# Kernel optimization log

Hardware: AMD Instinct MI355X
Metric: run time of the kernel (lower is better)

The kernel has to match this reference:

```python
import jax, jax.numpy as jnp
import numpy as np

EPS = 1e-5

def ln(x, w, b):
    mu = jnp.mean(x, axis=-1, keepdims=True)
    var = jnp.mean(jnp.square(x - mu), axis=-1, keepdims=True)
    return (x - mu) * jax.lax.rsqrt(var + EPS) * w + b

def setup_inputs() -> dict:
    key = jax.random.key(0)
    ks = jax.random.split(key, 4)
    B, H, W, C = 8, 224, 224, 96
    Cout = 2 * C  # 192
    x = jax.random.normal(ks[0], (B, H, W, C), dtype=jnp.float32)
    saliency_map = jax.random.uniform(ks[1], (B, H, W), dtype=jnp.float32)
    # PatchMerging reduction: Linear(4C -> 2C, bias=False), xavier_uniform init
    limit = float(np.sqrt(6.0 / (4 * C + Cout)))
    merge_w = jax.random.uniform(ks[2], (Cout, 4 * C), minval=-limit, maxval=limit, dtype=jnp.float32)
    return {
        "x": x,
        "saliency_map": saliency_map,
        "merge_w": merge_w,
        "merge_norm_w": jnp.ones((4 * C,), jnp.float32),
        "merge_norm_b": jnp.zeros((4 * C,), jnp.float32),
        "vss_norm_w": jnp.ones((Cout,), jnp.float32),
        "vss_norm_b": jnp.zeros((Cout,), jnp.float32),
        "asram_norm_w": jnp.ones((Cout,), jnp.float32),
        "asram_norm_b": jnp.zeros((Cout,), jnp.float32),
        "final_norm_w": jnp.ones((Cout,), jnp.float32),
        "final_norm_b": jnp.zeros((Cout,), jnp.float32),
    }

def reference(x, saliency_map, merge_w, merge_norm_w, merge_norm_b,
              vss_norm_w, vss_norm_b, asram_norm_w, asram_norm_b,
              final_norm_w, final_norm_b):
    # --- PatchMerging: [B,H,W,C] -> [B,H/2,W/2,2C] ---
    x0 = x[:, 0::2, 0::2, :]
    x1 = x[:, 1::2, 0::2, :]
    x2 = x[:, 0::2, 1::2, :]
    x3 = x[:, 1::2, 1::2, :]
    xm = jnp.concatenate([x0, x1, x2, x3], axis=-1)          # [B,H/2,W/2,4C]
    xm = ln(xm, merge_norm_w, merge_norm_b)
    xs = jnp.einsum('bhwi,oi->bhwo', xm, merge_w)            # [B,H/2,W/2,2C]
    # saliency adaptation (bilinear resize, align_corners=False); mock ASRAM ignores it
    B, Hn, Wn, _ = xs.shape
    _sal = jax.image.resize(saliency_map[:, None], (B, 1, Hn, Wn), method='bilinear')
    del _sal  # unused by mock ASRAM, kept for fidelity of the dataflow
    # --- Mock DualVSSBlock: x + LayerNorm(x) ---
    xv = xs + ln(xs, vss_norm_w, vss_norm_b)
    # --- Mock ASRAM: LayerNorm over channels (permute round-trip is a no-op here) ---
    xa = ln(xv, asram_norm_w, asram_norm_b)
    # --- Final LayerNorm ---
    return ln(xa, final_norm_w, final_norm_b)
```

## Files before the change

kernel.cpp:

```cpp
#include <hip/hip_runtime.h>
#include <cstdint>
#include <cstddef>

typedef float f32x4  __attribute__((ext_vector_type(4)));
typedef short bf16x8 __attribute__((ext_vector_type(8)));
typedef int   i32x4  __attribute__((ext_vector_type(4)));

#define LN_EPS 1e-5f

static __device__ __forceinline__ unsigned short f2bf(float f) {
    unsigned int u = __float_as_uint(f);
    u += 0x7fffu + ((u >> 16) & 1u);
    return (unsigned short)(u >> 16);
}
static __device__ __forceinline__ float bf2f(unsigned short h) {
    return __uint_as_float(((unsigned int)h) << 16);
}

__global__ void prep_w_kernel(const float* __restrict__ W,
                              unsigned short* __restrict__ wsh) {
    int o = blockIdx.x * 256 + threadIdx.x;
    if (o >= 192 * 384) return;
    int j    = o & 7;
    int lane = (o >> 3) & 63;
    int t    = o >> 9;
    int nf   = t % 12;
    int kk   = t / 12;
    int n = nf * 16 + (lane & 15);
    int k = kk * 32 + (lane >> 4) * 8 + j;
    wsh[o] = f2bf(W[n * 384 + k]);
}

template <bool USE_WS>
__global__ __launch_bounds__(256, 3)
void fused_kernel(const float* __restrict__ x,
                  const unsigned short* __restrict__ wsh,
                  const float* __restrict__ Wf,
                  const float* __restrict__ mw, const float* __restrict__ mb,
                  const float* __restrict__ vw, const float* __restrict__ vb,
                  const float* __restrict__ aw, const float* __restrict__ ab,
                  const float* __restrict__ fw, const float* __restrict__ fb,
                  float* __restrict__ out) {
    __shared__ __align__(16) unsigned char lds[49152];

    const int tid = threadIdx.x;
    const int r   = tid >> 3;
    const int u   = tid & 7;
    const int q   = u >> 1;
    const int hh  = u & 1;

    const int wv = tid >> 6;
    const int l  = tid & 63;
    const int g  = l >> 4;
    const int cl = l & 15;

    {
        const int R   = blockIdx.x * 32 + r;
        const int b   = R / 12544;
        const int rem = R - b * 12544;
        const int h2  = rem / 112;
        const int w2  = rem - h2 * 112;
        const int h   = 2 * h2 + (q & 1);
        const int w   = 2 * w2 + (q >> 1);
        const f32x4* src = (const f32x4*)(x + (((size_t)b * 224 + h) * 224 + w) * 96 + hh * 48);
        f32x4 v[12];
        #pragma unroll
        for (int i = 0; i < 12; i++) v[i] = src[i];

        float s = 0.f;
        #pragma unroll
        for (int i = 0; i < 12; i++) {
            #pragma unroll
            for (int e = 0; e < 4; e++) s += v[i][e];
        }
        s += __shfl_xor(s, 1); s += __shfl_xor(s, 2); s += __shfl_xor(s, 4);
        const float mu = s * (1.f / 384.f);
        float sd = 0.f;
        #pragma unroll
        for (int i = 0; i < 12; i++) {
            #pragma unroll
            for (int e = 0; e < 4; e++) { float d = v[i][e] - mu; sd += d * d; }
        }
        sd += __shfl_xor(sd, 1); sd += __shfl_xor(sd, 2); sd += __shfl_xor(sd, 4);
        const float rs = rsqrtf(sd * (1.f / 384.f) + LN_EPS);

        const f32x4* mwv = (const f32x4*)(mw + q * 96 + hh * 48);
        const f32x4* mbv = (const f32x4*)(mb + q * 96 + hh * 48);
        #pragma unroll
        for (int p = 0; p < 6; p++) {
            union { unsigned short u16[8]; i32x4 v4; } ph, pl;
            #pragma unroll
            for (int half = 0; half < 2; half++) {
                const int i = 2 * p + half;
                f32x4 w4 = mwv[i], b4 = mbv[i];
                #pragma unroll
                for (int e = 0; e < 4; e++) {
                    float a = (v[i][e] - mu) * rs * w4[e] + b4[e];
                    unsigned short hi = f2bf(a);
                    ph.u16[4 * half + e] = hi;
                    pl.u16[4 * half + e] = f2bf(a - bf2f(hi));
                }
            }
            const int slot = 6 * u + p;
            const int boff = (slot * 16) ^ ((r & 7) << 4);
            *(i32x4*)(&lds[r * 768 + boff])         = ph.v4;
            *(i32x4*)(&lds[24576 + r * 768 + boff]) = pl.v4;
        }
    }
    __syncthreads();

    f32x4 acc[2][3];
    #pragma unroll
    for (int mf = 0; mf < 2; mf++)
        #pragma unroll
        for (int t = 0; t < 3; t++) acc[mf][t] = (f32x4){0.f, 0.f, 0.f, 0.f};

    if (USE_WS) {
        #pragma unroll
        for (int half = 0; half < 2; half++) {
            bf16x8 B[6][3];
            #pragma unroll
            for (int kx = 0; kx < 6; kx++) {
                const int kk = 6 * half + kx;
                const bf16x8* bp = (const bf16x8*)wsh + ((kk * 12 + 3 * wv) * 64 + l);
                B[kx][0] = bp[0]; B[kx][1] = bp[64]; B[kx][2] = bp[128];
            }
            #pragma unroll
            for (int kx = 0; kx < 6; kx++) {
                asm volatile("" : "+v"(B[kx][0]), "+v"(B[kx][1]), "+v"(B[kx][2]));
            }
            #pragma unroll
            for (int kx = 0; kx < 6; kx++) {
                const int kk = 6 * half + kx;
                #pragma unroll
                for (int mf = 0; mf < 2; mf++) {
                    const int row  = 16 * mf + cl;
                    const int boff = (kk * 64 + g * 16) ^ ((row & 7) << 4);
                    bf16x8 afh = *(const bf16x8*)(&lds[row * 768 + boff]);
                    bf16x8 afl = *(const bf16x8*)(&lds[24576 + row * 768 + boff]);
                    #pragma unroll
                    for (int t = 0; t < 3; t++) {
                        acc[mf][t] = __builtin_amdgcn_mfma_f32_16x16x32_bf16(afh, B[kx][t], acc[mf][t], 0, 0, 0);
                        acc[mf][t] = __builtin_amdgcn_mfma_f32_16x16x32_bf16(afl, B[kx][t], acc[mf][t], 0, 0, 0);
                    }
                }
            }
        }
    } else {
        #pragma unroll
        for (int kk = 0; kk < 12; kk++) {
            bf16x8 bh[3];
            #pragma unroll
            for (int t = 0; t < 3; t++) {
                const int n = (3 * wv + t) * 16 + cl;
                const float* wp = Wf + n * 384 + kk * 32 + g * 8;
                f32x4 lo = *(const f32x4*)wp;
                f32x4 hi4 = *(const f32x4*)(wp + 4);
                bf16x8 hbb;
                #pragma unroll
                for (int e = 0; e < 4; e++) {
                    hbb[e] = (short)f2bf(lo[e]); hbb[4 + e] = (short)f2bf(hi4[e]);
                }
                bh[t] = hbb;
            }
            #pragma unroll
            for (int mf = 0; mf < 2; mf++) {
                const int row  = 16 * mf + cl;
                const int boff = (kk * 64 + g * 16) ^ ((row & 7) << 4);
                bf16x8 afh = *(const bf16x8*)(&lds[row * 768 + boff]);
                bf16x8 afl = *(const bf16x8*)(&lds[24576 + row * 768 + boff]);
                #pragma unroll
                for (int t = 0; t < 3; t++) {
                    acc[mf][t] = __builtin_amdgcn_mfma_f32_16x16x32_bf16(afh, bh[t], acc[mf][t], 0, 0, 0);
                    acc[mf][t] = __builtin_amdgcn_mfma_f32_16x16x32_bf16(afl, bh[t], acc[mf][t], 0, 0, 0);
                }
            }
        }
    }
    __syncthreads();

    {
        float* xsl = (float*)lds;
        #pragma unroll
        for (int mf = 0; mf < 2; mf++)
            #pragma unroll
            for (int t = 0; t < 3; t++) {
                const int col = 48 * wv + 16 * t + cl;
                #pragma unroll
                for (int rg = 0; rg < 4; rg++) {
                    const int row = 16 * mf + 4 * g + rg;
                    xsl[row * 196 + col] = acc[mf][t][rg];
                }
            }
    }
    __syncthreads();

    {
        const float* rowp = (const float*)lds + r * 196 + u * 24;
        float vv[24];
        #pragma unroll
        for (int i = 0; i < 6; i++) {
            f32x4 t4 = *(const f32x4*)(rowp + 4 * i);
            #pragma unroll
            for (int e = 0; e < 4; e++) vv[4 * i + e] = t4[e];
        }
        float s1 = 0.f;
        #pragma unroll
        for (int i = 0; i < 24; i++) s1 += vv[i];
        s1 += __shfl_xor(s1, 1); s1 += __shfl_xor(s1, 2); s1 += __shfl_xor(s1, 4);
        const float mu1 = s1 * (1.f / 192.f);
        float d1 = 0.f;
        #pragma unroll
        for (int i = 0; i < 24; i++) { float d = vv[i] - mu1; d1 += d * d; }
        d1 += __shfl_xor(d1, 1); d1 += __shfl_xor(d1, 2); d1 += __shfl_xor(d1, 4);
        const float r1 = rsqrtf(d1 * (1.f / 192.f) + LN_EPS);

        const f32x4* vwv = (const f32x4*)(vw + u * 24);
        const f32x4* vbv = (const f32x4*)(vb + u * 24);
        float s2 = 0.f;
        #pragma unroll
        for (int i = 0; i < 6; i++) {
            f32x4 w4 = vwv[i], b4 = vbv[i];
            #pragma unroll
            for (int e = 0; e < 4; e++) {
                float xs0 = vv[4 * i + e];
                float xv0 = xs0 + (xs0 - mu1) * r1 * w4[e] + b4[e];
                vv[4 * i + e] = xv0;
                s2 += xv0;
            }
        }
        s2 += __shfl_xor(s2, 1); s2 += __shfl_xor(s2, 2); s2 += __shfl_xor(s2, 4);
        const float mu2 = s2 * (1.f / 192.f);
        float d2 = 0.f;
        #pragma unroll
        for (int i = 0; i < 24; i++) { float d = vv[i] - mu2; d2 += d * d; }
        d2 += __shfl_xor(d2, 1); d2 += __shfl_xor(d2, 2); d2 += __shfl_xor(d2, 4);
        const float r2 = rsqrtf(d2 * (1.f / 192.f) + LN_EPS);

        const f32x4* awv = (const f32x4*)(aw + u * 24);
        const f32x4* abv = (const f32x4*)(ab + u * 24);
        float s3 = 0.f;
        #pragma unroll
        for (int i = 0; i < 6; i++) {
            f32x4 w4 = awv[i], b4 = abv[i];
            #pragma unroll
            for (int e = 0; e < 4; e++) {
                float xa0 = (vv[4 * i + e] - mu2) * r2 * w4[e] + b4[e];
                vv[4 * i + e] = xa0;
                s3 += xa0;
            }
        }
        s3 += __shfl_xor(s3, 1); s3 += __shfl_xor(s3, 2); s3 += __shfl_xor(s3, 4);
        const float mu3 = s3 * (1.f / 192.f);
        float d3 = 0.f;
        #pragma unroll
        for (int i = 0; i < 24; i++) { float d = vv[i] - mu3; d3 += d * d; }
        d3 += __shfl_xor(d3, 1); d3 += __shfl_xor(d3, 2); d3 += __shfl_xor(d3, 4);
        const float r3 = rsqrtf(d3 * (1.f / 192.f) + LN_EPS);

        const f32x4* fwv = (const f32x4*)(fw + u * 24);
        const f32x4* fbv = (const f32x4*)(fb + u * 24);
        float* op = out + (size_t)(blockIdx.x * 32 + r) * 192 + u * 24;
        #pragma unroll
        for (int i = 0; i < 6; i++) {
            f32x4 w4 = fwv[i], b4 = fbv[i];
            f32x4 o4;
            #pragma unroll
            for (int e = 0; e < 4; e++)
                o4[e] = (vv[4 * i + e] - mu3) * r3 * w4[e] + b4[e];
            *(f32x4*)(op + 4 * i) = o4;
        }
    }
}

extern "C" void kernel_launch(void* const* d_in, const int* in_sizes, int n_in,
                              void* d_out, int out_size, void* d_ws, size_t ws_size,
                              hipStream_t stream) {
    const float* x  = (const float*)d_in[0];
    const float* W  = (const float*)d_in[2];
    const float* mw = (const float*)d_in[3];
    const float* mb = (const float*)d_in[4];
    const float* vw = (const float*)d_in[5];
    const float* vb = (const float*)d_in[6];
    const float* aw = (const float*)d_in[7];
    const float* ab = (const float*)d_in[8];
    const float* fw = (const float*)d_in[9];
    const float* fb = (const float*)d_in[10];
    float* out = (float*)d_out;

    const int rows   = 8 * 112 * 112;
    const int blocks = rows / 32;

    unsigned short* wsh = (unsigned short*)d_ws;

    if (ws_size >= (size_t)(192 * 384 * 2)) {
        prep_w_kernel<<<288, 256, 0, stream>>>(W, wsh);
        fused_kernel<true><<<blocks, 256, 0, stream>>>(x, wsh, W, mw, mb, vw, vb,
                                                       aw, ab, fw, fb, out);
    } else {
        fused_kernel<false><<<blocks, 256, 0, stream>>>(x, wsh, W, mw, mb, vw, vb,
                                                        aw, ab, fw, fb, out);
    }
}
```

Baseline: 87.70 us.

## Fold merge LayerNorm affine into GEMM weights and apply normalization post-GEMM

The merge LayerNorm gamma is folded into the bf16 weights, and per-output constants (W·gamma, W·beta) are precomputed by a new small kernel. Raw x is split into hi/lo bf16 and written to LDS before the mean/variance are computed, so the LDS store no longer waits on the reduction. Normalization is applied after the GEMM as rs*(acc - mu*s2) + c0. This trades an extra tiny kernel launch and a possible precision change (cancellation on raw, un-centered inputs) for less per-element work before the GEMM. The bf16 conversion is also switched to the HIP intrinsic.

```diff
diff --git a/kernel.cpp b/kernel.cpp
--- a/kernel.cpp
+++ b/kernel.cpp
@@ -1,4 +1,5 @@
 #include <hip/hip_runtime.h>
+#include <hip/hip_bf16.h>
 #include <cstdint>
 #include <cstddef>
 
@@ -9,15 +10,16 @@
 #define LN_EPS 1e-5f
 
 static __device__ __forceinline__ unsigned short f2bf(float f) {
-    unsigned int u = __float_as_uint(f);
-    u += 0x7fffu + ((u >> 16) & 1u);
-    return (unsigned short)(u >> 16);
+    __hip_bfloat16 h = __float2bfloat16(f);
+    union { __hip_bfloat16 b; unsigned short u; } cv; cv.b = h;
+    return cv.u;
 }
 static __device__ __forceinline__ float bf2f(unsigned short h) {
     return __uint_as_float(((unsigned int)h) << 16);
 }
 
 __global__ void prep_w_kernel(const float* __restrict__ W,
+                              const float* __restrict__ g,
                               unsigned short* __restrict__ wsh) {
     int o = blockIdx.x * 256 + threadIdx.x;
     if (o >= 192 * 384) return;
@@ -28,13 +30,27 @@
     int kk   = t / 12;
     int n = nf * 16 + (lane & 15);
     int k = kk * 32 + (lane >> 4) * 8 + j;
-    wsh[o] = f2bf(W[n * 384 + k]);
+    wsh[o] = f2bf(g[k] * W[n * 384 + k]);
+}
+
+__global__ void prep_sc_kernel(const float* __restrict__ W,
+                               const float* __restrict__ g,
+                               const float* __restrict__ b,
+                               float* __restrict__ s2,
+                               float* __restrict__ c0) {
+    int o = threadIdx.x;
+    if (o >= 192) return;
+    const float* wr = W + o * 384;
+    float a = 0.f, c = 0.f;
+    for (int i = 0; i < 384; i++) { float w = wr[i]; a += g[i] * w; c += b[i] * w; }
+    s2[o] = a; c0[o] = c;
 }
 
 template <bool USE_WS>
 __global__ __launch_bounds__(256, 3)
 void fused_kernel(const float* __restrict__ x,
                   const unsigned short* __restrict__ wsh,
+                  const float* __restrict__ s2p, const float* __restrict__ c0p,
                   const float* __restrict__ Wf,
                   const float* __restrict__ mw, const float* __restrict__ mb,
                   const float* __restrict__ vw, const float* __restrict__ vb,
@@ -53,6 +69,8 @@
     const int l  = tid & 63;
     const int g  = l >> 4;
     const int cl = l & 15;
+
+    float mu = 0.f, rs = 0.f;
 
     {
         const int R   = blockIdx.x * 32 + r;
@@ -67,44 +85,82 @@
         #pragma unroll
         for (int i = 0; i < 12; i++) v[i] = src[i];
 
-        float s = 0.f;
-        #pragma unroll
-        for (int i = 0; i < 12; i++) {
-            #pragma unroll
-            for (int e = 0; e < 4; e++) s += v[i][e];
-        }
-        s += __shfl_xor(s, 1); s += __shfl_xor(s, 2); s += __shfl_xor(s, 4);
-        const float mu = s * (1.f / 384.f);
-        float sd = 0.f;
-        #pragma unroll
-        for (int i = 0; i < 12; i++) {
-            #pragma unroll
-            for (int e = 0; e < 4; e++) { float d = v[i][e] - mu; sd += d * d; }
-        }
-        sd += __shfl_xor(sd, 1); sd += __shfl_xor(sd, 2); sd += __shfl_xor(sd, 4);
-        const float rs = rsqrtf(sd * (1.f / 384.f) + LN_EPS);
-
-        const f32x4* mwv = (const f32x4*)(mw + q * 96 + hh * 48);
-        const f32x4* mbv = (const f32x4*)(mb + q * 96 + hh * 48);
-        #pragma unroll
-        for (int p = 0; p < 6; p++) {
-            union { unsigned short u16[8]; i32x4 v4; } ph, pl;
-            #pragma unroll
-            for (int half = 0; half < 2; half++) {
-                const int i = 2 * p + half;
-                f32x4 w4 = mwv[i], b4 = mbv[i];
-                #pragma unroll
-                for (int e = 0; e < 4; e++) {
-                    float a = (v[i][e] - mu) * rs * w4[e] + b4[e];
-                    unsigned short hi = f2bf(a);
-                    ph.u16[4 * half + e] = hi;
-                    pl.u16[4 * half + e] = f2bf(a - bf2f(hi));
-                }
-            }
-            const int slot = 6 * u + p;
-            const int boff = (slot * 16) ^ ((r & 7) << 4);
-            *(i32x4*)(&lds[r * 768 + boff])         = ph.v4;
-            *(i32x4*)(&lds[24576 + r * 768 + boff]) = pl.v4;
+        if (USE_WS) {
+            #pragma unroll
+            for (int p = 0; p < 6; p++) {
+                union { unsigned short u16[8]; i32x4 v4; } ph, pl;
+                #pragma unroll
+                for (int half = 0; half < 2; half++) {
+                    const int i = 2 * p + half;
+                    #pragma unroll
+                    for (int e = 0; e < 4; e++) {
+                        float a = v[i][e];
+                        unsigned short hi = f2bf(a);
+                        ph.u16[4 * half + e] = hi;
+                        pl.u16[4 * half + e] = f2bf(a - bf2f(hi));
+                    }
+                }
+                const int slot = 6 * u + p;
+                const int boff = (slot * 16) ^ ((r & 7) << 4);
+                *(i32x4*)(&lds[r * 768 + boff])         = ph.v4;
+                *(i32x4*)(&lds[24576 + r * 768 + boff]) = pl.v4;
+            }
+            float s = 0.f;
+            #pragma unroll
+            for (int i = 0; i < 12; i++) {
+                #pragma unroll
+                for (int e = 0; e < 4; e++) s += v[i][e];
+            }
+            s += __shfl_xor(s, 1); s += __shfl_xor(s, 2); s += __shfl_xor(s, 4);
+            mu = s * (1.f / 384.f);
+            float sd = 0.f;
+            #pragma unroll
+            for (int i = 0; i < 12; i++) {
+                #pragma unroll
+                for (int e = 0; e < 4; e++) { float d = v[i][e] - mu; sd += d * d; }
+            }
+            sd += __shfl_xor(sd, 1); sd += __shfl_xor(sd, 2); sd += __shfl_xor(sd, 4);
+            rs = rsqrtf(sd * (1.f / 384.f) + LN_EPS);
+        } else {
+            float s = 0.f;
+            #pragma unroll
+            for (int i = 0; i < 12; i++) {
+                #pragma unroll
+                for (int e = 0; e < 4; e++) s += v[i][e];
+            }
+            s += __shfl_xor(s, 1); s += __shfl_xor(s, 2); s += __shfl_xor(s, 4);
+            mu = s * (1.f / 384.f);
+            float sd = 0.f;
+            #pragma unroll
+            for (int i = 0; i < 12; i++) {
+                #pragma unroll
+                for (int e = 0; e < 4; e++) { float d = v[i][e] - mu; sd += d * d; }
+            }
+            sd += __shfl_xor(sd, 1); sd += __shfl_xor(sd, 2); sd += __shfl_xor(sd, 4);
+            rs = rsqrtf(sd * (1.f / 384.f) + LN_EPS);
+
+            const f32x4* mwv = (const f32x4*)(mw + q * 96 + hh * 48);
+            const f32x4* mbv = (const f32x4*)(mb + q * 96 + hh * 48);
+            #pragma unroll
+            for (int p = 0; p < 6; p++) {
+                union { unsigned short u16[8]; i32x4 v4; } ph, pl;
+                #pragma unroll
+                for (int half = 0; half < 2; half++) {
+                    const int i = 2 * p + half;
+                    f32x4 w4 = mwv[i], b4 = mbv[i];
+                    #pragma unroll
+                    for (int e = 0; e < 4; e++) {
+                        float a = (v[i][e] - mu) * rs * w4[e] + b4[e];
+                        unsigned short hi = f2bf(a);
+                        ph.u16[4 * half + e] = hi;
+                        pl.u16[4 * half + e] = f2bf(a - bf2f(hi));
+                    }
+                }
+                const int slot = 6 * u + p;
+                const int boff = (slot * 16) ^ ((r & 7) << 4);
+                *(i32x4*)(&lds[r * 768 + boff])         = ph.v4;
+                *(i32x4*)(&lds[24576 + r * 768 + boff]) = pl.v4;
+            }
         }
     }
     __syncthreads();
@@ -204,6 +260,17 @@
             #pragma unroll
             for (int e = 0; e < 4; e++) vv[4 * i + e] = t4[e];
         }
+        if (USE_WS) {
+            const f32x4* s2v = (const f32x4*)(s2p + u * 24);
+            const f32x4* c0v = (const f32x4*)(c0p + u * 24);
+            #pragma unroll
+            for (int i = 0; i < 6; i++) {
+                f32x4 sv = s2v[i], cv = c0v[i];
+                #pragma unroll
+                for (int e = 0; e < 4; e++)
+                    vv[4 * i + e] = rs * (vv[4 * i + e] - mu * sv[e]) + cv[e];
+            }
+        }
         float s1 = 0.f;
         #pragma unroll
         for (int i = 0; i < 24; i++) s1 += vv[i];
@@ -217,7 +284,7 @@
 
         const f32x4* vwv = (const f32x4*)(vw + u * 24);
         const f32x4* vbv = (const f32x4*)(vb + u * 24);
-        float s2 = 0.f;
+        float s2s = 0.f;
         #pragma unroll
         for (int i = 0; i < 6; i++) {
             f32x4 w4 = vwv[i], b4 = vbv[i];
@@ -226,11 +293,11 @@
                 float xs0 = vv[4 * i + e];
                 float xv0 = xs0 + (xs0 - mu1) * r1 * w4[e] + b4[e];
                 vv[4 * i + e] = xv0;
-                s2 += xv0;
-            }
-        }
-        s2 += __shfl_xor(s2, 1); s2 += __shfl_xor(s2, 2); s2 += __shfl_xor(s2, 4);
-        const float mu2 = s2 * (1.f / 192.f);
+                s2s += xv0;
+            }
+        }
+        s2s += __shfl_xor(s2s, 1); s2s += __shfl_xor(s2s, 2); s2s += __shfl_xor(s2s, 4);
+        const float mu2 = s2s * (1.f / 192.f);
         float d2 = 0.f;
         #pragma unroll
         for (int i = 0; i < 24; i++) { float d = vv[i] - mu2; d2 += d * d; }
@@ -292,13 +359,16 @@
     const int blocks = rows / 32;
 
     unsigned short* wsh = (unsigned short*)d_ws;
-
-    if (ws_size >= (size_t)(192 * 384 * 2)) {
-        prep_w_kernel<<<288, 256, 0, stream>>>(W, wsh);
-        fused_kernel<true><<<blocks, 256, 0, stream>>>(x, wsh, W, mw, mb, vw, vb,
-                                                       aw, ab, fw, fb, out);
+    float* s2 = (float*)((char*)d_ws + 192 * 384 * 2);
+    float* c0 = s2 + 192;
+
+    if (ws_size >= (size_t)(192 * 384 * 2 + 2 * 192 * 4)) {
+        prep_w_kernel<<<288, 256, 0, stream>>>(W, mw, wsh);
+        prep_sc_kernel<<<1, 192, 0, stream>>>(W, mw, mb, s2, c0);
+        fused_kernel<true><<<blocks, 256, 0, stream>>>(x, wsh, s2, c0, W, mw, mb,
+                                                       vw, vb, aw, ab, fw, fb, out);
     } else {
-        fused_kernel<false><<<blocks, 256, 0, stream>>>(x, wsh, W, mw, mb, vw, vb,
-                                                        aw, ab, fw, fb, out);
-    }
-}
+        fused_kernel<false><<<blocks, 256, 0, stream>>>(x, wsh, s2, c0, W, mw, mb,
+                                                        vw, vb, aw, ab, fw, fb, out);
+    }
+}
```

Measured after the change: 90.65 us. 1.03x slower.
